# Kernel optimization log

Measured on AMD Instinct MI355X. Metric: run time of the kernel, lower is better.

## Reference

```python
import jax, jax.numpy as jnp
import numpy as np

D_MODEL = 1024
N_HEAD = 16
D_K = D_MODEL // N_HEAD


def setup_inputs() -> dict:
    key = jax.random.key(0)
    ks = jax.random.split(key, 12)
    B, S = 2, 2048
    s = 1.0 / np.sqrt(D_MODEL)
    return {
        "query": jax.random.normal(ks[0], (B, S, D_MODEL), jnp.float32),
        "key": jax.random.normal(ks[1], (B, S, D_MODEL), jnp.float32),
        "value": jax.random.normal(ks[2], (B, S, D_MODEL), jnp.float32),
        "Wq": jax.random.normal(ks[3], (D_MODEL, D_MODEL), jnp.float32) * s,
        "bq": jnp.zeros((D_MODEL,), jnp.float32),
        "Wk": jax.random.normal(ks[4], (D_MODEL, D_MODEL), jnp.float32) * s,
        "bk": jnp.zeros((D_MODEL,), jnp.float32),
        "Wv": jax.random.normal(ks[5], (D_MODEL, D_MODEL), jnp.float32) * s,
        "bv": jnp.zeros((D_MODEL,), jnp.float32),
        "Wo": jax.random.normal(ks[6], (D_MODEL, D_MODEL), jnp.float32) * s,
        "bo": jnp.zeros((D_MODEL,), jnp.float32),
    }


def reference(query, key, value, Wq, bq, Wk, bk, Wv, bv, Wo, bo):
    B, S, _ = query.shape
    # QKV projections (torch Linear: x @ W.T + b)
    q = query @ Wq.T + bq
    k = key @ Wk.T + bk
    v = value @ Wv.T + bv
    # [B, S, H, Dk] -> [B, H, S, Dk]
    q = q.reshape(B, S, N_HEAD, D_K).transpose(0, 2, 1, 3)
    k = k.reshape(B, -1, N_HEAD, D_K).transpose(0, 2, 1, 3)
    v = v.reshape(B, -1, N_HEAD, D_K).transpose(0, 2, 1, 3)
    # scores [B, H, Sq, Sk]
    attn = jnp.einsum("bhqd,bhkd->bhqk", q, k) / jnp.sqrt(jnp.float32(D_K))
    attn = jax.nn.softmax(attn, axis=-1)  # dropout p=0 -> identity
    out = jnp.einsum("bhqk,bhkd->bhqd", attn, v)
    out = out.transpose(0, 2, 1, 3).reshape(B, S, D_MODEL)
    return out @ Wo.T + bo
```

## Files before the change

kernel.cpp:

```cpp
#include <hip/hip_runtime.h>
#include <cstdint>
#include <cstddef>

#define DM 1024
#define NHEAD 16
#define DKH 64
#define SEQLEN 2048
#define NBATCH 2
#define MTOT (NBATCH * SEQLEN)

typedef __attribute__((ext_vector_type(8))) short bf16x8;
typedef __attribute__((ext_vector_type(4))) float f32x4;
typedef __attribute__((ext_vector_type(16))) float f32x16;
typedef __attribute__((ext_vector_type(2))) unsigned int u32x2;

#define QSCALE 0.18033688011112042f

__device__ __forceinline__ uint16_t f2bf(float f) {
  uint32_t x = __float_as_uint(f);
  uint32_t r = x + 0x7FFFu + ((x >> 16) & 1u);
  return (uint16_t)(r >> 16);
}

__device__ __forceinline__ uint32_t cvtpk(float a, float b) {
  uint32_t r;
  asm("v_cvt_pk_bf16_f32 %0, %1, %2" : "=v"(r) : "v"(a), "v"(b));
  return r;
}

__device__ __forceinline__ float exp2_fast(float x) {
  float r;
  asm("v_exp_f32 %0, %1" : "=v"(r) : "v"(x));
  return r;
}

__device__ __forceinline__ float max3f(float a, float b, float c) {
  float r;
  asm("v_max3_f32 %0, %1, %2, %3" : "=v"(r) : "v"(a), "v"(b), "v"(c));
  return r;
}

__device__ __forceinline__ void gload_lds16(const void* g, void* l) {
  __builtin_amdgcn_global_load_lds(
      (const __attribute__((address_space(1))) void*)g,
      (__attribute__((address_space(3))) void*)l, 16, 0, 0);
}

__device__ __forceinline__ int fsw(int r) { return ((r + (r >> 3)) & 7) << 4; }

struct CvtArgs {
  const float* src[7];
  uint16_t* dst[7];
  int end4[7];
};

__global__ void cvt_all_kernel(CvtArgs a) {
  int i = blockIdx.x * blockDim.x + threadIdx.x;
  int r = 0;
#pragma unroll
  for (int j = 0; j < 7; ++j)
    if (i >= a.end4[j]) r = j + 1;
  if (r >= 7) return;
  int local = i - (r == 0 ? 0 : a.end4[r - 1]);
  float4 v = reinterpret_cast<const float4*>(a.src[r])[local];
  uint64_t p = (uint64_t)f2bf(v.x) | ((uint64_t)f2bf(v.y) << 16) |
               ((uint64_t)f2bf(v.z) << 32) | ((uint64_t)f2bf(v.w) << 48);
  reinterpret_cast<uint64_t*>(a.dst[r])[local] = p;
}

__global__ __launch_bounds__(256)
void gemm_qkv(const uint16_t* __restrict__ xq, const uint16_t* __restrict__ xk,
              const uint16_t* __restrict__ xv, const uint16_t* __restrict__ wqkv,
              const float* __restrict__ bqp, const float* __restrict__ bkp,
              const float* __restrict__ bvp, uint16_t* __restrict__ Qp,
              uint16_t* __restrict__ Kp, uint16_t* __restrict__ VTp) {
  __shared__ uint16_t smem[2 * 128 * 64];
  const int tid = threadIdx.x;
  const int wave = tid >> 6, lane = tid & 63;
  const int l15 = lane & 15, l4 = lane >> 4;
  const int proj = blockIdx.y >> 3;
  const int brow = blockIdx.x * 128, bcol = (blockIdx.y & 7) * 128;
  const int wr = (wave >> 1) * 64, wc = (wave & 1) * 64;
  const uint16_t* A = proj == 0 ? xq : proj == 1 ? xk : xv;
  const uint16_t* Bt = wqkv + (size_t)proj * DM * DM;
  const float* bias = proj == 0 ? bqp : proj == 1 ? bkp : bvp;

  const f32x4 fzero = {0.f, 0.f, 0.f, 0.f};
  f32x4 acc[4][4];
#pragma unroll
  for (int m = 0; m < 4; ++m)
#pragma unroll
    for (int n = 0; n < 4; ++n) acc[m][n] = fzero;

  for (int k0 = 0; k0 < DM; k0 += 64) {
#pragma unroll
    for (int t = 0; t < 8; ++t) {
      const int o = t * 4096 + wave * 1024 + lane * 16;
      const uint16_t* g;
      if (t < 4) {
        const int row = o >> 7, kk = (o & 127) >> 1;
        g = A + (size_t)(brow + row) * DM + (k0 + kk);
      } else {
        const int o2 = o - 16384;
        const int row = o2 >> 7, kk = (o2 & 127) >> 1;
        g = Bt + (size_t)(bcol + row) * DM + (k0 + kk);
      }
      gload_lds16(g, (char*)smem + t * 4096 + wave * 1024);
    }
    __syncthreads();
    const uint16_t* At = smem;
    const uint16_t* Bs = smem + 128 * 64;
#pragma unroll
    for (int ks = 0; ks < 2; ++ks) {
      bf16x8 a[4], b[4];
#pragma unroll
      for (int m = 0; m < 4; ++m)
        a[m] = *(const bf16x8*)(At + (wr + m * 16 + l15) * 64 + ks * 32 + l4 * 8);
#pragma unroll
      for (int n = 0; n < 4; ++n)
        b[n] = *(const bf16x8*)(Bs + (wc + n * 16 + l15) * 64 + ks * 32 + l4 * 8);
#pragma unroll
      for (int m = 0; m < 4; ++m)
#pragma unroll
        for (int n = 0; n < 4; ++n)
          acc[m][n] = __builtin_amdgcn_mfma_f32_16x16x32_bf16(a[m], b[n], acc[m][n], 0, 0, 0);
    }
    __syncthreads();
  }

  const float scale = proj == 0 ? QSCALE : 1.0f;
  uint16_t* dstQK = proj == 0 ? Qp : Kp;
#pragma unroll
  for (int m = 0; m < 4; ++m) {
#pragma unroll
    for (int n = 0; n < 4; ++n) {
      const int gcol = bcol + wc + n * 16 + l15;
      const float bv = bias[gcol];
      if (proj == 2) {
        const int grow0 = brow + wr + m * 16 + l4 * 4;
        const int b_ = grow0 >> 11, s_ = grow0 & 2047;
        const int h_ = gcol >> 6, d_ = gcol & 63;
        uint16_t* dst = VTp + ((size_t)((b_ * NHEAD + h_) * DKH + d_)) * SEQLEN + s_;
        uint64_t pk = (uint64_t)f2bf(acc[m][n][0] + bv) |
                      ((uint64_t)f2bf(acc[m][n][1] + bv) << 16) |
                      ((uint64_t)f2bf(acc[m][n][2] + bv) << 32) |
                      ((uint64_t)f2bf(acc[m][n][3] + bv) << 48);
        *(uint64_t*)dst = pk;
      } else {
#pragma unroll
        for (int r = 0; r < 4; ++r) {
          const int grow = brow + wr + m * 16 + l4 * 4 + r;
          dstQK[(size_t)grow * DM + gcol] = f2bf((acc[m][n][r] + bv) * scale);
        }
      }
    }
  }
}

__global__ __launch_bounds__(256)
void gemm_out(const uint16_t* __restrict__ A, const uint16_t* __restrict__ Bt,
              const float* __restrict__ bias, float* __restrict__ C) {
  __shared__ uint16_t smem[2 * 128 * 64];
  const int tid = threadIdx.x;
  const int wave = tid >> 6, lane = tid & 63;
  const int l15 = lane & 15, l4 = lane >> 4;
  const int brow = blockIdx.x * 128, bcol = blockIdx.y * 128;
  const int wr = (wave >> 1) * 64, wc = (wave & 1) * 64;

  const f32x4 fzero = {0.f, 0.f, 0.f, 0.f};
  f32x4 acc[4][4];
#pragma unroll
  for (int m = 0; m < 4; ++m)
#pragma unroll
    for (int n = 0; n < 4; ++n) acc[m][n] = fzero;

  for (int k0 = 0; k0 < DM; k0 += 64) {
#pragma unroll
    for (int t = 0; t < 8; ++t) {
      const int o = t * 4096 + wave * 1024 + lane * 16;
      const uint16_t* g;
      if (t < 4) {
        const int row = o >> 7, kk = (o & 127) >> 1;
        g = A + (size_t)(brow + row) * DM + (k0 + kk);
      } else {
        const int o2 = o - 16384;
        const int row = o2 >> 7, kk = (o2 & 127) >> 1;
        g = Bt + (size_t)(bcol + row) * DM + (k0 + kk);
      }
      gload_lds16(g, (char*)smem + t * 4096 + wave * 1024);
    }
    __syncthreads();
    const uint16_t* At = smem;
    const uint16_t* Bs = smem + 128 * 64;
#pragma unroll
    for (int ks = 0; ks < 2; ++ks) {
      bf16x8 a[4], b[4];
#pragma unroll
      for (int m = 0; m < 4; ++m)
        a[m] = *(const bf16x8*)(At + (wr + m * 16 + l15) * 64 + ks * 32 + l4 * 8);
#pragma unroll
      for (int n = 0; n < 4; ++n)
        b[n] = *(const bf16x8*)(Bs + (wc + n * 16 + l15) * 64 + ks * 32 + l4 * 8);
#pragma unroll
      for (int m = 0; m < 4; ++m)
#pragma unroll
        for (int n = 0; n < 4; ++n)
          acc[m][n] = __builtin_amdgcn_mfma_f32_16x16x32_bf16(a[m], b[n], acc[m][n], 0, 0, 0);
    }
    __syncthreads();
  }

#pragma unroll
  for (int m = 0; m < 4; ++m) {
#pragma unroll
    for (int n = 0; n < 4; ++n) {
      const int gcol = bcol + wc + n * 16 + l15;
      const float bv = bias[gcol];
#pragma unroll
      for (int r = 0; r < 4; ++r) {
        const int grow = brow + wr + m * 16 + l4 * 4 + r;
        C[(size_t)grow * DM + gcol] = acc[m][n][r] + bv;
      }
    }
  }
}

__device__ __forceinline__ void stage_kv(const uint16_t* __restrict__ Kg,
                                         const uint16_t* __restrict__ Vg,
                                         char* buf, int wave, int lane) {
#pragma unroll
  for (int i = 0; i < 2; ++i) {
    const int base = i * 4096 + wave * 1024;
    const int row = i * 32 + wave * 8 + (lane >> 3);
    const int esw = (((lane & 7) << 4) ^ fsw(row)) >> 1;
    gload_lds16(Kg + (size_t)row * DM + esw, buf + base);
    gload_lds16(Vg + (size_t)row * SEQLEN + esw, buf + 8192 + base);
  }
}

__global__ __launch_bounds__(256)
void attn_fwd_kernel(const uint16_t* __restrict__ Qp, const uint16_t* __restrict__ Kp,
                     const uint16_t* __restrict__ VTp, uint16_t* __restrict__ Op) {
  __shared__ __align__(16) char lds[32768];
  const int tid = threadIdx.x;
  const int wave = tid >> 6, lane = tid & 63;
  const int l31 = lane & 31, hi = lane >> 5;
  const int bb = blockIdx.z, h = blockIdx.y;
  const int q0 = blockIdx.x * 128;

  const int qrow = q0 + wave * 32 + l31;
  const uint16_t* qb = Qp + ((size_t)(bb * SEQLEN + qrow)) * DM + h * DKH;
  bf16x8 qf[4];
#pragma unroll
  for (int ds = 0; ds < 4; ++ds)
    qf[ds] = *(const bf16x8*)(qb + ds * 16 + hi * 8);

  bf16x8 onesf;
#pragma unroll
  for (int j = 0; j < 8; ++j) onesf[j] = (short)0x3F80;

  f32x16 oacc[2], lacc;
#pragma unroll
  for (int m = 0; m < 2; ++m)
#pragma unroll
    for (int r = 0; r < 16; ++r) oacc[m][r] = 0.f;
#pragma unroll
  for (int r = 0; r < 16; ++r) lacc[r] = 0.f;
  float mrow = -1e30f;

  const uint16_t* Kg = Kp + ((size_t)(bb * SEQLEN)) * DM + h * DKH;
  const uint16_t* Vg = VTp + ((size_t)((bb * NHEAD + h) * DKH)) * SEQLEN;

  stage_kv(Kg, Vg, lds, wave, lane);

  const int NT = SEQLEN / 64;
  for (int t = 0; t < NT; ++t) {
    __syncthreads();
    if (t + 1 < NT)
      stage_kv(Kg + (size_t)(t + 1) * 64 * DM, Vg + (t + 1) * 64,
               lds + ((t + 1) & 1) * 16384, wave, lane);
    const char* kb = lds + (t & 1) * 16384;
    const char* vb = kb + 8192;

    f32x16 sacc[2];
#pragma unroll
    for (int n = 0; n < 2; ++n)
#pragma unroll
      for (int r = 0; r < 16; ++r) sacc[n][r] = 0.f;
    __builtin_amdgcn_s_setprio(1);
#pragma unroll
    for (int n = 0; n < 2; ++n) {
      const int kr = 32 * n + l31;
      const char* krow = kb + kr * 128;
      const int f = fsw(kr);
#pragma unroll
      for (int ds = 0; ds < 4; ++ds) {
        const bf16x8 kf = *(const bf16x8*)(krow + ((ds * 32 + hi * 16) ^ f));
        sacc[n] = __builtin_amdgcn_mfma_f32_32x32x16_bf16(kf, qf[ds], sacc[n], 0, 0, 0);
      }
    }
    __builtin_amdgcn_s_setprio(0);

    float ma = max3f(sacc[0][0], sacc[0][1], sacc[0][2]);
    ma = max3f(ma, sacc[0][3], sacc[0][4]);
    ma = max3f(ma, sacc[0][5], sacc[0][6]);
    ma = max3f(ma, sacc[0][7], sacc[0][8]);
    ma = max3f(ma, sacc[0][9], sacc[0][10]);
    ma = max3f(ma, sacc[0][11], sacc[0][12]);
    ma = max3f(ma, sacc[0][13], sacc[0][14]);
    float mb = max3f(sacc[1][0], sacc[1][1], sacc[1][2]);
    mb = max3f(mb, sacc[1][3], sacc[1][4]);
    mb = max3f(mb, sacc[1][5], sacc[1][6]);
    mb = max3f(mb, sacc[1][7], sacc[1][8]);
    mb = max3f(mb, sacc[1][9], sacc[1][10]);
    mb = max3f(mb, sacc[1][11], sacc[1][12]);
    mb = max3f(mb, sacc[1][13], sacc[1][14]);
    float mx = max3f(fmaxf(ma, sacc[0][15]), mb, sacc[1][15]);
    mx = fmaxf(mx, __shfl_xor(mx, 32, 64));

    float mnew = mrow;
    if (__any(mx > mrow + 8.f)) {
      mnew = fmaxf(mrow, mx);
      const float scl = exp2_fast(mrow - mnew);
#pragma unroll
      for (int m = 0; m < 2; ++m)
#pragma unroll
        for (int r = 0; r < 16; ++r) oacc[m][r] *= scl;
      lacc[0] *= scl;
    }
    mrow = mnew;

#pragma unroll
    for (int n = 0; n < 2; ++n) {
      float pv[16];
#pragma unroll
      for (int r = 0; r < 16; ++r) pv[r] = exp2_fast(sacc[n][r] - mnew);
      const uint32_t c0 = cvtpk(pv[0], pv[1]),   c1 = cvtpk(pv[2], pv[3]);
      const uint32_t c2 = cvtpk(pv[4], pv[5]),   c3 = cvtpk(pv[6], pv[7]);
      const uint32_t c4 = cvtpk(pv[8], pv[9]),   c5 = cvtpk(pv[10], pv[11]);
      const uint32_t c6 = cvtpk(pv[12], pv[13]), c7 = cvtpk(pv[14], pv[15]);
      const u32x2 r02 = __builtin_amdgcn_permlane32_swap(c0, c2, false, false);
      const u32x2 r13 = __builtin_amdgcn_permlane32_swap(c1, c3, false, false);
      const u32x2 r46 = __builtin_amdgcn_permlane32_swap(c4, c6, false, false);
      const u32x2 r57 = __builtin_amdgcn_permlane32_swap(c5, c7, false, false);
      union { uint32_t w[4]; bf16x8 v; } f0, f1;
      f0.w[0] = r02.x; f0.w[1] = r13.x; f0.w[2] = r02.y; f0.w[3] = r13.y;
      f1.w[0] = r46.x; f1.w[1] = r57.x; f1.w[2] = r46.y; f1.w[3] = r57.y;

      __builtin_amdgcn_s_setprio(1);
#pragma unroll
      for (int m = 0; m < 2; ++m) {
        const int vr = 32 * m + l31;
        const char* vrow = vb + vr * 128;
        const int f = fsw(vr);
        const bf16x8 v0 = *(const bf16x8*)(vrow + ((n * 64 + hi * 16) ^ f));
        const bf16x8 v1 = *(const bf16x8*)(vrow + ((n * 64 + 32 + hi * 16) ^ f));
        oacc[m] = __builtin_amdgcn_mfma_f32_32x32x16_bf16(v0, f0.v, oacc[m], 0, 0, 0);
        oacc[m] = __builtin_amdgcn_mfma_f32_32x32x16_bf16(v1, f1.v, oacc[m], 0, 0, 0);
      }
      lacc = __builtin_amdgcn_mfma_f32_32x32x16_bf16(onesf, f0.v, lacc, 0, 0, 0);
      lacc = __builtin_amdgcn_mfma_f32_32x32x16_bf16(onesf, f1.v, lacc, 0, 0, 0);
      __builtin_amdgcn_s_setprio(0);
    }
  }

  const float il = 1.0f / lacc[0];
  uint16_t* ob = Op + ((size_t)(bb * SEQLEN + qrow)) * DM + h * DKH;
#pragma unroll
  for (int m = 0; m < 2; ++m)
#pragma unroll
    for (int rq = 0; rq < 4; ++rq) {
      const uint32_t w0 = cvtpk(oacc[m][4 * rq + 0] * il, oacc[m][4 * rq + 1] * il);
      const uint32_t w1 = cvtpk(oacc[m][4 * rq + 2] * il, oacc[m][4 * rq + 3] * il);
      *(uint64_t*)(ob + 32 * m + 8 * rq + 4 * hi) =
          (uint64_t)w0 | ((uint64_t)w1 << 32);
    }
}

extern "C" void kernel_launch(void* const* d_in, const int* in_sizes, int n_in,
                              void* d_out, int out_size, void* d_ws, size_t ws_size,
                              hipStream_t stream) {
  (void)in_sizes; (void)n_in; (void)out_size; (void)ws_size;
  const float* query = (const float*)d_in[0];
  const float* key_i = (const float*)d_in[1];
  const float* value = (const float*)d_in[2];
  const float* Wq = (const float*)d_in[3];
  const float* bq = (const float*)d_in[4];
  const float* Wk = (const float*)d_in[5];
  const float* bk = (const float*)d_in[6];
  const float* Wv = (const float*)d_in[7];
  const float* bv = (const float*)d_in[8];
  const float* Wo = (const float*)d_in[9];
  const float* bo = (const float*)d_in[10];
  float* out = (float*)d_out;

  char* ws = (char*)d_ws;
  const size_t MB = 1ull << 20;
  uint16_t* xq  = (uint16_t*)(ws + 0 * MB);
  uint16_t* xk  = (uint16_t*)(ws + 8 * MB);
  uint16_t* xv  = (uint16_t*)(ws + 16 * MB);
  uint16_t* wqkv = (uint16_t*)(ws + 24 * MB);
  uint16_t* wob = (uint16_t*)(ws + 30 * MB);
  uint16_t* Qp  = (uint16_t*)(ws + 32 * MB);
  uint16_t* Kp  = (uint16_t*)(ws + 40 * MB);
  uint16_t* VTp = (uint16_t*)(ws + 48 * MB);
  uint16_t* AO  = (uint16_t*)(ws + 56 * MB);

  const int n4x = (MTOT * DM) / 4;
  const int n4w = (DM * DM) / 4;
  CvtArgs ca;
  ca.src[0] = query; ca.dst[0] = xq;
  ca.src[1] = key_i; ca.dst[1] = xk;
  ca.src[2] = value; ca.dst[2] = xv;
  ca.src[3] = Wq;    ca.dst[3] = wqkv;
  ca.src[4] = Wk;    ca.dst[4] = wqkv + DM * DM;
  ca.src[5] = Wv;    ca.dst[5] = wqkv + 2 * DM * DM;
  ca.src[6] = Wo;    ca.dst[6] = wob;
  int acc = 0;
  for (int j = 0; j < 7; ++j) { acc += (j < 3) ? n4x : n4w; ca.end4[j] = acc; }
  const int blk = 256;
  cvt_all_kernel<<<(acc + blk - 1) / blk, blk, 0, stream>>>(ca);

  dim3 gq(MTOT / 128, 24);
  gemm_qkv<<<gq, 256, 0, stream>>>(xq, xk, xv, wqkv, bq, bk, bv, Qp, Kp, VTp);

  dim3 ga(SEQLEN / 128, NHEAD, NBATCH);
  attn_fwd_kernel<<<ga, 256, 0, stream>>>(Qp, Kp, VTp, AO);

  dim3 gg(MTOT / 128, DM / 128);
  gemm_out<<<gg, 256, 0, stream>>>(AO, wob, bo, out);
}
```

Before: 153.7 us.

## Double-buffer LDS tiles in QKV and output projection GEMMs

Both projection GEMMs now allocate two LDS tile buffers. The next K-slice's global-to-LDS load is issued before the MFMA compute on the current slice, and one of the two barriers per iteration is dropped. The goal is to overlap global memory latency with matrix-core work. In exchange, LDS use per block doubles to 64 KB, which may reduce how many blocks fit per CU. The async LDS loads may also be forced to complete early by compiler-inserted waits, which would limit the overlap.

```diff
diff --git a/kernel.cpp b/kernel.cpp
--- a/kernel.cpp
+++ b/kernel.cpp
@@ -68,13 +68,33 @@
   reinterpret_cast<uint64_t*>(a.dst[r])[local] = p;
 }
 
+__device__ __forceinline__ void gemm_stage(const uint16_t* __restrict__ A,
+                                           const uint16_t* __restrict__ Bt,
+                                           int brow, int bcol, int k0,
+                                           char* smem, int buf, int wave, int lane) {
+#pragma unroll
+  for (int t = 0; t < 8; ++t) {
+    const int o = t * 4096 + wave * 1024 + lane * 16;
+    const uint16_t* g;
+    if (t < 4) {
+      const int row = o >> 7, kk = (o & 127) >> 1;
+      g = A + (size_t)(brow + row) * DM + (k0 + kk);
+    } else {
+      const int o2 = o - 16384;
+      const int row = o2 >> 7, kk = (o2 & 127) >> 1;
+      g = Bt + (size_t)(bcol + row) * DM + (k0 + kk);
+    }
+    gload_lds16(g, smem + buf * 32768 + t * 4096 + wave * 1024);
+  }
+}
+
 __global__ __launch_bounds__(256)
 void gemm_qkv(const uint16_t* __restrict__ xq, const uint16_t* __restrict__ xk,
               const uint16_t* __restrict__ xv, const uint16_t* __restrict__ wqkv,
               const float* __restrict__ bqp, const float* __restrict__ bkp,
               const float* __restrict__ bvp, uint16_t* __restrict__ Qp,
               uint16_t* __restrict__ Kp, uint16_t* __restrict__ VTp) {
-  __shared__ uint16_t smem[2 * 128 * 64];
+  __shared__ uint16_t smem[2 * 2 * 128 * 64];
   const int tid = threadIdx.x;
   const int wave = tid >> 6, lane = tid & 63;
   const int l15 = lane & 15, l4 = lane >> 4;
@@ -92,24 +112,14 @@
 #pragma unroll
     for (int n = 0; n < 4; ++n) acc[m][n] = fzero;
 
+  gemm_stage(A, Bt, brow, bcol, 0, (char*)smem, 0, wave, lane);
+  int cur = 0;
   for (int k0 = 0; k0 < DM; k0 += 64) {
-#pragma unroll
-    for (int t = 0; t < 8; ++t) {
-      const int o = t * 4096 + wave * 1024 + lane * 16;
-      const uint16_t* g;
-      if (t < 4) {
-        const int row = o >> 7, kk = (o & 127) >> 1;
-        g = A + (size_t)(brow + row) * DM + (k0 + kk);
-      } else {
-        const int o2 = o - 16384;
-        const int row = o2 >> 7, kk = (o2 & 127) >> 1;
-        g = Bt + (size_t)(bcol + row) * DM + (k0 + kk);
-      }
-      gload_lds16(g, (char*)smem + t * 4096 + wave * 1024);
-    }
     __syncthreads();
-    const uint16_t* At = smem;
-    const uint16_t* Bs = smem + 128 * 64;
+    if (k0 + 64 < DM)
+      gemm_stage(A, Bt, brow, bcol, k0 + 64, (char*)smem, cur ^ 1, wave, lane);
+    const uint16_t* At = smem + cur * 16384;
+    const uint16_t* Bs = At + 8192;
 #pragma unroll
     for (int ks = 0; ks < 2; ++ks) {
       bf16x8 a[4], b[4];
@@ -125,7 +135,7 @@
         for (int n = 0; n < 4; ++n)
           acc[m][n] = __builtin_amdgcn_mfma_f32_16x16x32_bf16(a[m], b[n], acc[m][n], 0, 0, 0);
     }
-    __syncthreads();
+    cur ^= 1;
   }
 
   const float scale = proj == 0 ? QSCALE : 1.0f;
@@ -160,7 +170,7 @@
 __global__ __launch_bounds__(256)
 void gemm_out(const uint16_t* __restrict__ A, const uint16_t* __restrict__ Bt,
               const float* __restrict__ bias, float* __restrict__ C) {
-  __shared__ uint16_t smem[2 * 128 * 64];
+  __shared__ uint16_t smem[2 * 2 * 128 * 64];
   const int tid = threadIdx.x;
   const int wave = tid >> 6, lane = tid & 63;
   const int l15 = lane & 15, l4 = lane >> 4;
@@ -174,24 +184,14 @@
 #pragma unroll
     for (int n = 0; n < 4; ++n) acc[m][n] = fzero;
 
+  gemm_stage(A, Bt, brow, bcol, 0, (char*)smem, 0, wave, lane);
+  int cur = 0;
   for (int k0 = 0; k0 < DM; k0 += 64) {
-#pragma unroll
-    for (int t = 0; t < 8; ++t) {
-      const int o = t * 4096 + wave * 1024 + lane * 16;
-      const uint16_t* g;
-      if (t < 4) {
-        const int row = o >> 7, kk = (o & 127) >> 1;
-        g = A + (size_t)(brow + row) * DM + (k0 + kk);
-      } else {
-        const int o2 = o - 16384;
-        const int row = o2 >> 7, kk = (o2 & 127) >> 1;
-        g = Bt + (size_t)(bcol + row) * DM + (k0 + kk);
-      }
-      gload_lds16(g, (char*)smem + t * 4096 + wave * 1024);
-    }
     __syncthreads();
-    const uint16_t* At = smem;
-    const uint16_t* Bs = smem + 128 * 64;
+    if (k0 + 64 < DM)
+      gemm_stage(A, Bt, brow, bcol, k0 + 64, (char*)smem, cur ^ 1, wave, lane);
+    const uint16_t* At = smem + cur * 16384;
+    const uint16_t* Bs = At + 8192;
 #pragma unroll
     for (int ks = 0; ks < 2; ++ks) {
       bf16x8 a[4], b[4];
@@ -207,7 +207,7 @@
         for (int n = 0; n < 4; ++n)
           acc[m][n] = __builtin_amdgcn_mfma_f32_16x16x32_bf16(a[m], b[n], acc[m][n], 0, 0, 0);
     }
-    __syncthreads();
+    cur ^= 1;
   }
 
 #pragma unroll
```

Result: faster. 131.3 us (-14.6%).
